# Kernel tuning notes

Hardware: AMD Instinct MI355X
Metric: run time of the kernel (lower is better)

The kernel has to match this reference:

```python
import jax, jax.numpy as jnp
import numpy as np

N = 30000          # nodes
R = 8              # relations
NUM_BASES = 30     # basis decomposition (fixed in module)
IN_DIM = 256
Z_DIM = 128
HID = Z_DIM * 2
E = N * 16         # edges (avg degree 16)


def setup_inputs() -> dict:
    key = jax.random.key(0)
    ks = jax.random.split(key, 12)
    x = jax.random.normal(ks[0], (N, IN_DIM), jnp.float32)
    edge_index = jax.random.randint(ks[1], (2, E), 0, N, dtype=jnp.int64)
    edge_type = jax.random.randint(ks[2], (E,), 0, R, dtype=jnp.int64)
    s1 = 1.0 / np.sqrt(IN_DIM)
    s2 = 1.0 / np.sqrt(HID)
    sb = 1.0 / np.sqrt(NUM_BASES)
    bases1 = jax.random.normal(ks[3], (NUM_BASES, IN_DIM, HID), jnp.float32) * s1
    comp1 = jax.random.normal(ks[4], (R, NUM_BASES), jnp.float32) * sb
    root1 = jax.random.normal(ks[5], (IN_DIM, HID), jnp.float32) * s1
    bias1 = jnp.zeros((HID,), jnp.float32)
    bases2 = jax.random.normal(ks[6], (NUM_BASES, HID, Z_DIM), jnp.float32) * s2
    comp2 = jax.random.normal(ks[7], (R, NUM_BASES), jnp.float32) * sb
    root2 = jax.random.normal(ks[8], (HID, Z_DIM), jnp.float32) * s2
    bias2 = jnp.zeros((Z_DIM,), jnp.float32)
    return dict(x=x, edge_index=edge_index, edge_type=edge_type,
                bases1=bases1, comp1=comp1, root1=root1, bias1=bias1,
                bases2=bases2, comp2=comp2, root2=root2, bias2=bias2)


def _rgcn_layer(x, src, dst, etype, bases, comp, root, bias):
    # weight[r] = sum_b comp[r,b] * bases[b]  (basis decomposition)
    n = x.shape[0]
    W = jnp.einsum('rb,bio->rio', comp, bases)          # [R, in, out]
    xall = jnp.einsum('ni,rio->nro', x, W)              # [N, R, out] dense transform
    msg = xall[src, etype]                              # [E, out] gather per edge
    seg = dst * R + etype                               # segment = (dst, relation)
    sums = jax.ops.segment_sum(msg, seg, num_segments=n * R)
    cnt = jax.ops.segment_sum(jnp.ones((msg.shape[0],), msg.dtype), seg,
                              num_segments=n * R)
    mean = sums / jnp.maximum(cnt, 1.0)[:, None]        # PyG RGCNConv aggr='mean'
    agg = mean.reshape(n, R, -1).sum(axis=1)            # sum over relations
    return agg + x @ root + bias


def reference(x, edge_index, edge_type, bases1, comp1, root1, bias1,
              bases2, comp2, root2, bias2):
    src, dst = edge_index[0], edge_index[1]
    z = _rgcn_layer(x, src, dst, edge_type, bases1, comp1, root1, bias1)
    z = jax.nn.leaky_relu(z, negative_slope=0.01)
    z = _rgcn_layer(z, src, dst, edge_type, bases2, comp2, root2, bias2)
    return z
```

## Files before the change

kernel.cpp:

```cpp
#include <hip/hip_runtime.h>
#include <hip/hip_bf16.h>
#include <stdint.h>

#define NN     30000
#define MPAD   30080
#define RR     8
#define NBASES 30
#define KD     256
#define EE     480000
#define NSEG   (NN * RR)
#define BK     64
#define CAP    32
#define NC1    2304
#define NC2    1152

typedef unsigned short u16;
typedef __attribute__((ext_vector_type(8))) short bf16x8;
typedef __attribute__((ext_vector_type(4))) float f32x4;

__device__ __forceinline__ u16 f2b(float f) {
  union { float f; uint32_t u; } v; v.f = f;
  return (u16)((v.u + 0x7fffu + ((v.u >> 16) & 1u)) >> 16);
}
__device__ __forceinline__ float b2f(u16 h) {
  union { uint32_t u; float f; } v; v.u = ((uint32_t)h) << 16;
  return v.f;
}

__device__ __forceinline__ void gl_lds16(const void* g, void* l) {
  __builtin_amdgcn_global_load_lds((__attribute__((address_space(1))) void*)g,
                                   (__attribute__((address_space(3))) void*)l,
                                   16, 0, 0);
}

template<int NCOLS>
__global__ __launch_bounds__(512, 6)
void k_gemm_y(const u16* __restrict__ A, const u16* __restrict__ Bn,
              u16* __restrict__ Y) {
  constexpr int NT = 128;
  constexpr int NI = 4;
  constexpr int NKI = KD / BK;
  __shared__ __align__(16) char smem[49152];
  u16 (*Alds)[64 * BK] = (u16(*)[64 * BK])smem;
  u16 (*Blds)[NT * BK] = (u16(*)[NT * BK])(smem + 2 * 64 * BK * 2);
  float* eps = (float*)smem;
  const int tid = threadIdx.x;
  const int w = tid >> 6, lane = tid & 63;
  const int bn = blockIdx.x * NT, bm = blockIdx.y * 64;
  const int wm = (w >> 1) * 16;
  const int wn = (w & 1) * 64;
  const int l15 = lane & 15, l4 = lane >> 4;

  f32x4 acc[NI];
  #pragma unroll
  for (int ni = 0; ni < NI; ++ni) acc[ni] = (f32x4){0.f, 0.f, 0.f, 0.f};

  auto stage = [&](int buf, int k0) {
    {
      int chb = w * 64;
      int ch = chb + lane;
      int row = ch >> 3, pc = ch & 7;
      int lc = pc ^ (row & 7);
      gl_lds16(&A[(size_t)(bm + row) * KD + k0 + lc * 8], &Alds[buf][chb * 8]);
    }
    #pragma unroll
    for (int it = 0; it < 2; ++it) {
      int chb = it * 512 + w * 64;
      int ch = chb + lane;
      int row = ch >> 3, pc = ch & 7;
      int lc = pc ^ (row & 7);
      gl_lds16(&Bn[(size_t)(bn + row) * KD + k0 + lc * 8], &Blds[buf][chb * 8]);
    }
  };

  stage(0, 0);
  __syncthreads();
  int buf = 0;
  for (int t = 0; t < NKI; ++t) {
    if (t + 1 < NKI) stage(buf ^ 1, (t + 1) * BK);
    #pragma unroll
    for (int s = 0; s < 2; ++s) {
      bf16x8 av, bv[NI];
      {
        int row = wm + l15;
        int pc = (4 * s + l4) ^ (row & 7);
        av = *(const bf16x8*)&Alds[buf][row * BK + pc * 8];
      }
      #pragma unroll
      for (int ni = 0; ni < NI; ++ni) {
        int row = wn + ni * 16 + l15;
        int pc = (4 * s + l4) ^ (row & 7);
        bv[ni] = *(const bf16x8*)&Blds[buf][row * BK + pc * 8];
      }
      #pragma unroll
      for (int ni = 0; ni < NI; ++ni)
        acc[ni] = __builtin_amdgcn_mfma_f32_16x16x32_bf16(av, bv[ni], acc[ni], 0, 0, 0);
    }
    __syncthreads();
    buf ^= 1;
  }

  #pragma unroll
  for (int ni = 0; ni < NI; ++ni) {
    int col = wn + ni * 16 + l15;
    #pragma unroll
    for (int v = 0; v < 4; ++v) {
      int row = wm + l4 * 4 + v;
      eps[row * 132 + col] = acc[ni][v];
    }
  }
  __syncthreads();
  {
    int row = tid >> 3, oc = tid & 7;
    const float* src = &eps[row * 132 + oc * 16];
    uint4 o[2];
    #pragma unroll
    for (int h = 0; h < 2; ++h) {
      float f0 = src[h*8+0], f1 = src[h*8+1], f2 = src[h*8+2], f3 = src[h*8+3];
      float f4 = src[h*8+4], f5 = src[h*8+5], f6 = src[h*8+6], f7 = src[h*8+7];
      o[h].x = ((uint32_t)f2b(f1) << 16) | (uint32_t)f2b(f0);
      o[h].y = ((uint32_t)f2b(f3) << 16) | (uint32_t)f2b(f2);
      o[h].z = ((uint32_t)f2b(f5) << 16) | (uint32_t)f2b(f4);
      o[h].w = ((uint32_t)f2b(f7) << 16) | (uint32_t)f2b(f6);
    }
    u16* dst = &Y[(size_t)(bm + row) * NCOLS + bn + oc * 16];
    *(uint4*)dst = o[0];
    *(uint4*)(dst + 8) = o[1];
  }
}

template<int D, bool LAST>
__global__ __launch_bounds__(256)
void k_agg(const u16* __restrict__ Y, const int* __restrict__ cnt,
           const int* __restrict__ esrc, const float* __restrict__ bias,
           u16* __restrict__ ob, float* __restrict__ of) {
  constexpr int YW = 9 * D;
  constexpr int CW = D / 32;
  __shared__ float part[8 * D];
  const int d = blockIdx.x, tid = threadIdx.x;
  const int r = tid >> 5, ln = tid & 31;
  const int s = (d << 3) + r;
  int n = cnt[s]; n = n < CAP ? n : CAP;
  const int base = s * CAP;

  float a[CW];
  #pragma unroll
  for (int j = 0; j < CW; ++j) a[j] = 0.f;
  #pragma unroll 1
  for (int e = 0; e < n; ++e) {
    int sr = esrc[base + e];
    const u16* row = &Y[(size_t)sr * YW + r * D + ln * CW];
    if constexpr (CW == 8) {
      uint4 v = *(const uint4*)row;
      a[0] += b2f((u16)v.x); a[1] += b2f((u16)(v.x >> 16));
      a[2] += b2f((u16)v.y); a[3] += b2f((u16)(v.y >> 16));
      a[4] += b2f((u16)v.z); a[5] += b2f((u16)(v.z >> 16));
      a[6] += b2f((u16)v.w); a[7] += b2f((u16)(v.w >> 16));
    } else {
      uint2 v = *(const uint2*)row;
      a[0] += b2f((u16)v.x); a[1] += b2f((u16)(v.x >> 16));
      a[2] += b2f((u16)v.y); a[3] += b2f((u16)(v.y >> 16));
    }
  }
  float inv = (n > 0) ? 1.f / (float)n : 0.f;
  #pragma unroll
  for (int j = 0; j < CW; ++j) part[r * D + ln * CW + j] = a[j] * inv;
  __syncthreads();
  if (tid < D) {
    float v = 0.f;
    #pragma unroll
    for (int rr = 0; rr < 8; ++rr) v += part[rr * D + tid];
    v += b2f(Y[(size_t)d * YW + 8 * D + tid]);
    v += bias[tid];
    if (!LAST) {
      v = v > 0.f ? v : 0.01f * v;
      ob[(size_t)d * KD + tid] = f2b(v);
    } else {
      of[(size_t)d * D + tid] = v;
    }
  }
}

__global__ void k_cast_x(const float* __restrict__ x, u16* __restrict__ xb) {
  int t = blockIdx.x * 256 + threadIdx.x;
  if (t < NN * KD / 4) {
    float4 v = ((const float4*)x)[t];
    union { u16 h[4]; uint2 u; } p;
    p.h[0] = f2b(v.x); p.h[1] = f2b(v.y); p.h[2] = f2b(v.z); p.h[3] = f2b(v.w);
    ((uint2*)xb)[t] = p.u;
  }
}

__global__ void k_combineT1(const float* __restrict__ bases, const float* __restrict__ comp,
                            const float* __restrict__ root, u16* __restrict__ Bn) {
  int i = blockIdx.x, rg = blockIdx.y, o = threadIdx.x;
  float v; int j;
  if (rg < RR) {
    float acc = 0.f;
    #pragma unroll
    for (int b = 0; b < NBASES; ++b)
      acc += comp[rg * NBASES + b] * bases[(size_t)b * 65536 + i * 256 + o];
    v = acc; j = rg * 256 + o;
  } else {
    v = root[i * 256 + o]; j = 2048 + o;
  }
  Bn[(size_t)j * KD + i] = f2b(v);
}

__global__ void k_combineT2(const float* __restrict__ bases, const float* __restrict__ comp,
                            const float* __restrict__ root, u16* __restrict__ Bn) {
  int i = blockIdx.x, rg = blockIdx.y, o = threadIdx.x;
  float v; int j;
  if (rg < RR) {
    float acc = 0.f;
    #pragma unroll
    for (int b = 0; b < NBASES; ++b)
      acc += comp[rg * NBASES + b] * bases[(size_t)b * 32768 + i * 128 + o];
    v = acc; j = rg * 128 + o;
  } else {
    v = root[i * 128 + o]; j = 1024 + o;
  }
  Bn[(size_t)j * KD + i] = f2b(v);
}

__global__ void k_bucket_fs(const int* __restrict__ ei, const int* __restrict__ ety,
                            int* __restrict__ cnt, int* __restrict__ esrc) {
  int e = blockIdx.x * 256 + threadIdx.x;
  if (e < EE) {
    int seg = ei[EE + e] * RR + ety[e];
    int pos = atomicAdd(&cnt[seg], 1);
    if (pos < CAP) esrc[seg * CAP + pos] = ei[e];
  }
}

extern "C" void kernel_launch(void* const* d_in, const int* in_sizes, int n_in,
                              void* d_out, int out_size, void* d_ws, size_t ws_size,
                              hipStream_t stream) {
  const float* x      = (const float*)d_in[0];
  const int*   ei     = (const int*)d_in[1];
  const int*   ety    = (const int*)d_in[2];
  const float* bases1 = (const float*)d_in[3];
  const float* comp1  = (const float*)d_in[4];
  const float* root1  = (const float*)d_in[5];
  const float* bias1  = (const float*)d_in[6];
  const float* bases2 = (const float*)d_in[7];
  const float* comp2  = (const float*)d_in[8];
  const float* root2  = (const float*)d_in[9];
  const float* bias2  = (const float*)d_in[10];
  float* out = (float*)d_out;

  char* p = (char*)d_ws;
  auto alloc = [&](size_t bytes) {
    char* q = p; p += (bytes + 255) & ~(size_t)255; return q;
  };
  u16* Y    = (u16*)alloc((size_t)MPAD * NC1 * 2);
  u16* xb   = (u16*)alloc((size_t)MPAD * KD * 2);
  u16* z1b  = (u16*)alloc((size_t)MPAD * KD * 2);
  u16* Bn1  = (u16*)alloc((size_t)NC1 * KD * 2);
  u16* Bn2  = (u16*)alloc((size_t)NC2 * KD * 2);
  int* cnt  = (int*)alloc((size_t)NSEG * 4);
  int* esrc = (int*)alloc((size_t)NSEG * CAP * 4);

  hipMemsetAsync(cnt, 0, (size_t)NSEG * 4, stream);
  k_bucket_fs<<<(EE + 255) / 256, 256, 0, stream>>>(ei, ety, cnt, esrc);

  k_cast_x<<<NN * KD / 4 / 256, 256, 0, stream>>>(x, xb);
  k_combineT1<<<dim3(256, 9), 256, 0, stream>>>(bases1, comp1, root1, Bn1);
  k_combineT2<<<dim3(256, 9), 128, 0, stream>>>(bases2, comp2, root2, Bn2);

  k_gemm_y<NC1><<<dim3(NC1 / 128, 470), 512, 0, stream>>>(xb, Bn1, Y);
  k_agg<256, false><<<NN, 256, 0, stream>>>(Y, cnt, esrc, bias1, z1b, nullptr);

  k_gemm_y<NC2><<<dim3(NC2 / 128, 470), 512, 0, stream>>>(z1b, Bn2, Y);
  k_agg<128, true><<<NN, 256, 0, stream>>>(Y, cnt, esrc, bias2, nullptr, out);
}
```

Baseline: 374.4 us.

## Enlarge GEMM tiles to 128x128 and restructure aggregation to one half-wave per node

The per-relation GEMM tile grows from 64x128 to 128x128 so each wave issues 2x4 MFMAs per k-step. This improves reuse of the B tile, at the cost of 64KB of LDS, lower occupancy and an epilogue written out in two passes. The aggregation kernel now gives each 32-lane group a whole destination node. Each group loops over the 8 relations in registers, preloads counts and the first four source indices with vector loads, and unrolls those first gathers. This removes the LDS reduction and the block-wide barrier, and the final stores become vectorised.

```diff
diff --git a/kernel.cpp b/kernel.cpp
--- a/kernel.cpp
+++ b/kernel.cpp
@@ -34,30 +34,33 @@
 }
 
 template<int NCOLS>
-__global__ __launch_bounds__(512, 6)
+__global__ __launch_bounds__(512, 2)
 void k_gemm_y(const u16* __restrict__ A, const u16* __restrict__ Bn,
               u16* __restrict__ Y) {
-  constexpr int NT = 128;
-  constexpr int NI = 4;
+  constexpr int NT = 128, MT = 128;
+  constexpr int MI = 2, NI = 4;
   constexpr int NKI = KD / BK;
-  __shared__ __align__(16) char smem[49152];
-  u16 (*Alds)[64 * BK] = (u16(*)[64 * BK])smem;
-  u16 (*Blds)[NT * BK] = (u16(*)[NT * BK])(smem + 2 * 64 * BK * 2);
+  __shared__ __align__(16) char smem[65536];
+  u16 (*Alds)[MT * BK] = (u16(*)[MT * BK])smem;
+  u16 (*Blds)[NT * BK] = (u16(*)[NT * BK])(smem + 2 * MT * BK * 2);
   float* eps = (float*)smem;
   const int tid = threadIdx.x;
   const int w = tid >> 6, lane = tid & 63;
-  const int bn = blockIdx.x * NT, bm = blockIdx.y * 64;
-  const int wm = (w >> 1) * 16;
+  const int bn = blockIdx.x * NT, bm = blockIdx.y * MT;
+  const int wm = (w >> 1) * 32;
   const int wn = (w & 1) * 64;
   const int l15 = lane & 15, l4 = lane >> 4;
 
-  f32x4 acc[NI];
-  #pragma unroll
-  for (int ni = 0; ni < NI; ++ni) acc[ni] = (f32x4){0.f, 0.f, 0.f, 0.f};
+  f32x4 acc[MI][NI];
+  #pragma unroll
+  for (int mi = 0; mi < MI; ++mi)
+    #pragma unroll
+    for (int ni = 0; ni < NI; ++ni) acc[mi][ni] = (f32x4){0.f, 0.f, 0.f, 0.f};
 
   auto stage = [&](int buf, int k0) {
-    {
-      int chb = w * 64;
+    #pragma unroll
+    for (int it = 0; it < 2; ++it) {
+      int chb = it * 512 + w * 64;
       int ch = chb + lane;
       int row = ch >> 3, pc = ch & 7;
       int lc = pc ^ (row & 7);
@@ -80,11 +83,12 @@
     if (t + 1 < NKI) stage(buf ^ 1, (t + 1) * BK);
     #pragma unroll
     for (int s = 0; s < 2; ++s) {
-      bf16x8 av, bv[NI];
-      {
-        int row = wm + l15;
+      bf16x8 av[MI], bv[NI];
+      #pragma unroll
+      for (int mi = 0; mi < MI; ++mi) {
+        int row = wm + mi * 16 + l15;
         int pc = (4 * s + l4) ^ (row & 7);
-        av = *(const bf16x8*)&Alds[buf][row * BK + pc * 8];
+        av[mi] = *(const bf16x8*)&Alds[buf][row * BK + pc * 8];
       }
       #pragma unroll
       for (int ni = 0; ni < NI; ++ni) {
@@ -93,39 +97,49 @@
         bv[ni] = *(const bf16x8*)&Blds[buf][row * BK + pc * 8];
       }
       #pragma unroll
-      for (int ni = 0; ni < NI; ++ni)
-        acc[ni] = __builtin_amdgcn_mfma_f32_16x16x32_bf16(av, bv[ni], acc[ni], 0, 0, 0);
+      for (int mi = 0; mi < MI; ++mi)
+        #pragma unroll
+        for (int ni = 0; ni < NI; ++ni)
+          acc[mi][ni] = __builtin_amdgcn_mfma_f32_16x16x32_bf16(av[mi], bv[ni], acc[mi][ni], 0, 0, 0);
     }
     __syncthreads();
     buf ^= 1;
   }
 
   #pragma unroll
-  for (int ni = 0; ni < NI; ++ni) {
-    int col = wn + ni * 16 + l15;
-    #pragma unroll
-    for (int v = 0; v < 4; ++v) {
-      int row = wm + l4 * 4 + v;
-      eps[row * 132 + col] = acc[ni][v];
-    }
-  }
-  __syncthreads();
-  {
-    int row = tid >> 3, oc = tid & 7;
-    const float* src = &eps[row * 132 + oc * 16];
-    uint4 o[2];
-    #pragma unroll
-    for (int h = 0; h < 2; ++h) {
-      float f0 = src[h*8+0], f1 = src[h*8+1], f2 = src[h*8+2], f3 = src[h*8+3];
-      float f4 = src[h*8+4], f5 = src[h*8+5], f6 = src[h*8+6], f7 = src[h*8+7];
-      o[h].x = ((uint32_t)f2b(f1) << 16) | (uint32_t)f2b(f0);
-      o[h].y = ((uint32_t)f2b(f3) << 16) | (uint32_t)f2b(f2);
-      o[h].z = ((uint32_t)f2b(f5) << 16) | (uint32_t)f2b(f4);
-      o[h].w = ((uint32_t)f2b(f7) << 16) | (uint32_t)f2b(f6);
-    }
-    u16* dst = &Y[(size_t)(bm + row) * NCOLS + bn + oc * 16];
-    *(uint4*)dst = o[0];
-    *(uint4*)(dst + 8) = o[1];
+  for (int p = 0; p < 2; ++p) {
+    if ((wm >> 6) == p) {
+      #pragma unroll
+      for (int mi = 0; mi < MI; ++mi)
+        #pragma unroll
+        for (int ni = 0; ni < NI; ++ni) {
+          int col = wn + ni * 16 + l15;
+          #pragma unroll
+          for (int v = 0; v < 4; ++v) {
+            int row = (wm & 63) + mi * 16 + l4 * 4 + v;
+            eps[row * 132 + col] = acc[mi][ni][v];
+          }
+        }
+    }
+    __syncthreads();
+    {
+      int row = tid >> 3, oc = tid & 7;
+      const float* src = &eps[row * 132 + oc * 16];
+      uint4 o[2];
+      #pragma unroll
+      for (int hh = 0; hh < 2; ++hh) {
+        float f0 = src[hh*8+0], f1 = src[hh*8+1], f2 = src[hh*8+2], f3 = src[hh*8+3];
+        float f4 = src[hh*8+4], f5 = src[hh*8+5], f6 = src[hh*8+6], f7 = src[hh*8+7];
+        o[hh].x = ((uint32_t)f2b(f1) << 16) | (uint32_t)f2b(f0);
+        o[hh].y = ((uint32_t)f2b(f3) << 16) | (uint32_t)f2b(f2);
+        o[hh].z = ((uint32_t)f2b(f5) << 16) | (uint32_t)f2b(f4);
+        o[hh].w = ((uint32_t)f2b(f7) << 16) | (uint32_t)f2b(f6);
+      }
+      u16* dst = &Y[(size_t)(bm + p * 64 + row) * NCOLS + bn + oc * 16];
+      *(uint4*)dst = o[0];
+      *(uint4*)(dst + 8) = o[1];
+    }
+    __syncthreads();
   }
 }
 
@@ -136,47 +150,117 @@
            u16* __restrict__ ob, float* __restrict__ of) {
   constexpr int YW = 9 * D;
   constexpr int CW = D / 32;
-  __shared__ float part[8 * D];
-  const int d = blockIdx.x, tid = threadIdx.x;
-  const int r = tid >> 5, ln = tid & 31;
-  const int s = (d << 3) + r;
-  int n = cnt[s]; n = n < CAP ? n : CAP;
-  const int base = s * CAP;
+  const int tid = threadIdx.x;
+  const int h = tid >> 5, ln = tid & 31;
+  const int d = blockIdx.x * 8 + h;
+
+  int cn[8];
+  {
+    int4 c0 = *(const int4*)&cnt[d << 3];
+    int4 c1 = *(const int4*)&cnt[(d << 3) + 4];
+    cn[0]=c0.x; cn[1]=c0.y; cn[2]=c0.z; cn[3]=c0.w;
+    cn[4]=c1.x; cn[5]=c1.y; cn[6]=c1.z; cn[7]=c1.w;
+  }
+  int4 q[8];
+  #pragma unroll
+  for (int r = 0; r < 8; ++r)
+    q[r] = *(const int4*)&esrc[((d << 3) + r) * CAP];
 
   float a[CW];
   #pragma unroll
   for (int j = 0; j < CW; ++j) a[j] = 0.f;
-  #pragma unroll 1
-  for (int e = 0; e < n; ++e) {
-    int sr = esrc[base + e];
-    const u16* row = &Y[(size_t)sr * YW + r * D + ln * CW];
-    if constexpr (CW == 8) {
-      uint4 v = *(const uint4*)row;
-      a[0] += b2f((u16)v.x); a[1] += b2f((u16)(v.x >> 16));
-      a[2] += b2f((u16)v.y); a[3] += b2f((u16)(v.y >> 16));
-      a[4] += b2f((u16)v.z); a[5] += b2f((u16)(v.z >> 16));
-      a[6] += b2f((u16)v.w); a[7] += b2f((u16)(v.w >> 16));
+
+  #pragma unroll
+  for (int r = 0; r < 8; ++r) {
+    int n = cn[r] < CAP ? cn[r] : CAP;
+    if (n == 0) continue;
+    float t[CW];
+    #pragma unroll
+    for (int j = 0; j < CW; ++j) t[j] = 0.f;
+    const int qsrc[4] = {q[r].x, q[r].y, q[r].z, q[r].w};
+    #pragma unroll
+    for (int e = 0; e < 4; ++e) {
+      if (e < n) {
+        int sr = qsrc[e];
+        if constexpr (CW == 8) {
+          uint4 v = *(const uint4*)&Y[(size_t)sr * YW + r * D + ln * 8];
+          t[0]+=b2f((u16)v.x); t[1]+=b2f((u16)(v.x>>16));
+          t[2]+=b2f((u16)v.y); t[3]+=b2f((u16)(v.y>>16));
+          t[4]+=b2f((u16)v.z); t[5]+=b2f((u16)(v.z>>16));
+          t[6]+=b2f((u16)v.w); t[7]+=b2f((u16)(v.w>>16));
+        } else {
+          uint2 v = *(const uint2*)&Y[(size_t)sr * YW + r * D + ln * 4];
+          t[0]+=b2f((u16)v.x); t[1]+=b2f((u16)(v.x>>16));
+          t[2]+=b2f((u16)v.y); t[3]+=b2f((u16)(v.y>>16));
+        }
+      }
+    }
+    #pragma unroll 1
+    for (int e = 4; e < n; ++e) {
+      int sr = esrc[((d << 3) + r) * CAP + e];
+      if constexpr (CW == 8) {
+        uint4 v = *(const uint4*)&Y[(size_t)sr * YW + r * D + ln * 8];
+        t[0]+=b2f((u16)v.x); t[1]+=b2f((u16)(v.x>>16));
+        t[2]+=b2f((u16)v.y); t[3]+=b2f((u16)(v.y>>16));
+        t[4]+=b2f((u16)v.z); t[5]+=b2f((u16)(v.z>>16));
+        t[6]+=b2f((u16)v.w); t[7]+=b2f((u16)(v.w>>16));
+      } else {
+        uint2 v = *(const uint2*)&Y[(size_t)sr * YW + r * D + ln * 4];
+        t[0]+=b2f((u16)v.x); t[1]+=b2f((u16)(v.x>>16));
+        t[2]+=b2f((u16)v.y); t[3]+=b2f((u16)(v.y>>16));
+      }
+    }
+    float inv = 1.f / (float)n;
+    #pragma unroll
+    for (int j = 0; j < CW; ++j) a[j] = fmaf(inv, t[j], a[j]);
+  }
+
+  if constexpr (CW == 8) {
+    uint4 sv = *(const uint4*)&Y[(size_t)d * YW + 8 * D + ln * 8];
+    float s[8] = { b2f((u16)sv.x), b2f((u16)(sv.x>>16)),
+                   b2f((u16)sv.y), b2f((u16)(sv.y>>16)),
+                   b2f((u16)sv.z), b2f((u16)(sv.z>>16)),
+                   b2f((u16)sv.w), b2f((u16)(sv.w>>16)) };
+    float4 b0 = *(const float4*)&bias[ln * 8];
+    float4 b1 = *(const float4*)&bias[ln * 8 + 4];
+    float vv[8];
+    vv[0]=a[0]+s[0]+b0.x; vv[1]=a[1]+s[1]+b0.y;
+    vv[2]=a[2]+s[2]+b0.z; vv[3]=a[3]+s[3]+b0.w;
+    vv[4]=a[4]+s[4]+b1.x; vv[5]=a[5]+s[5]+b1.y;
+    vv[6]=a[6]+s[6]+b1.z; vv[7]=a[7]+s[7]+b1.w;
+    if (!LAST) {
+      #pragma unroll
+      for (int j = 0; j < 8; ++j) vv[j] = vv[j] > 0.f ? vv[j] : 0.01f * vv[j];
+      uint4 o;
+      o.x = ((uint32_t)f2b(vv[1]) << 16) | (uint32_t)f2b(vv[0]);
+      o.y = ((uint32_t)f2b(vv[3]) << 16) | (uint32_t)f2b(vv[2]);
+      o.z = ((uint32_t)f2b(vv[5]) << 16) | (uint32_t)f2b(vv[4]);
+      o.w = ((uint32_t)f2b(vv[7]) << 16) | (uint32_t)f2b(vv[6]);
+      *(uint4*)&ob[(size_t)d * KD + ln * 8] = o;
     } else {
-      uint2 v = *(const uint2*)row;
-      a[0] += b2f((u16)v.x); a[1] += b2f((u16)(v.x >> 16));
-      a[2] += b2f((u16)v.y); a[3] += b2f((u16)(v.y >> 16));
-    }
-  }
-  float inv = (n > 0) ? 1.f / (float)n : 0.f;
-  #pragma unroll
-  for (int j = 0; j < CW; ++j) part[r * D + ln * CW + j] = a[j] * inv;
-  __syncthreads();
-  if (tid < D) {
-    float v = 0.f;
-    #pragma unroll
-    for (int rr = 0; rr < 8; ++rr) v += part[rr * D + tid];
-    v += b2f(Y[(size_t)d * YW + 8 * D + tid]);
-    v += bias[tid];
+      float4 o0 = {vv[0], vv[1], vv[2], vv[3]};
+      float4 o1 = {vv[4], vv[5], vv[6], vv[7]};
+      *(float4*)&of[(size_t)d * 256 + ln * 8] = o0;
+      *(float4*)&of[(size_t)d * 256 + ln * 8 + 4] = o1;
+    }
+  } else {
+    uint2 sv = *(const uint2*)&Y[(size_t)d * YW + 8 * D + ln * 4];
+    float s[4] = { b2f((u16)sv.x), b2f((u16)(sv.x>>16)),
+                   b2f((u16)sv.y), b2f((u16)(sv.y>>16)) };
+    float4 b0 = *(const float4*)&bias[ln * 4];
+    float vv[4];
+    vv[0]=a[0]+s[0]+b0.x; vv[1]=a[1]+s[1]+b0.y;
+    vv[2]=a[2]+s[2]+b0.z; vv[3]=a[3]+s[3]+b0.w;
     if (!LAST) {
-      v = v > 0.f ? v : 0.01f * v;
-      ob[(size_t)d * KD + tid] = f2b(v);
+      #pragma unroll
+      for (int j = 0; j < 4; ++j) vv[j] = vv[j] > 0.f ? vv[j] : 0.01f * vv[j];
+      uint2 o;
+      o.x = ((uint32_t)f2b(vv[1]) << 16) | (uint32_t)f2b(vv[0]);
+      o.y = ((uint32_t)f2b(vv[3]) << 16) | (uint32_t)f2b(vv[2]);
+      *(uint2*)&ob[(size_t)d * KD + ln * 4] = o;
     } else {
-      of[(size_t)d * D + tid] = v;
+      float4 o = {vv[0], vv[1], vv[2], vv[3]};
+      *(float4*)&of[(size_t)d * 128 + ln * 4] = o;
     }
   }
 }
@@ -268,9 +352,9 @@
   k_combineT1<<<dim3(256, 9), 256, 0, stream>>>(bases1, comp1, root1, Bn1);
   k_combineT2<<<dim3(256, 9), 128, 0, stream>>>(bases2, comp2, root2, Bn2);
 
-  k_gemm_y<NC1><<<dim3(NC1 / 128, 470), 512, 0, stream>>>(xb, Bn1, Y);
-  k_agg<256, false><<<NN, 256, 0, stream>>>(Y, cnt, esrc, bias1, z1b, nullptr);
-
-  k_gemm_y<NC2><<<dim3(NC2 / 128, 470), 512, 0, stream>>>(z1b, Bn2, Y);
-  k_agg<128, true><<<NN, 256, 0, stream>>>(Y, cnt, esrc, bias2, nullptr, out);
-}
+  k_gemm_y<NC1><<<dim3(NC1 / 128, MPAD / 128), 512, 0, stream>>>(xb, Bn1, Y);
+  k_agg<256, false><<<NN / 8, 256, 0, stream>>>(Y, cnt, esrc, bias1, z1b, nullptr);
+
+  k_gemm_y<NC2><<<dim3(NC2 / 128, MPAD / 128), 512, 0, stream>>>(z1b, Bn2, Y);
+  k_agg<128, true><<<NN / 8, 256, 0, stream>>>(Y, cnt, esrc, bias2, nullptr, out);
+}
```

New measurement: 347.5 us. -7.2%, faster.
